# Kernel tuning notes

Measured on AMD Instinct MI355X. Metric: run time of the kernel, lower is better.

The kernel has to match this reference:

```python
import jax, jax.numpy as jnp
import numpy as np

N_NODES = 100000
N_EDGES = 1600000
D_IN = 256
D_OUT = 128


def setup_inputs() -> dict:
    key = jax.random.key(0)
    k1, k2, k3, k4, k5, k6 = jax.random.split(key, 6)
    x = jax.random.normal(k1, (N_NODES, D_IN), dtype=jnp.float32)
    src = jax.random.randint(k2, (N_EDGES,), 0, N_NODES, dtype=jnp.int64)
    dst = jnp.sort(jax.random.randint(k3, (N_EDGES,), 0, N_NODES, dtype=jnp.int64))
    w = jax.random.uniform(k4, (N_EDGES,), dtype=jnp.float32)
    # nn.Linear(input_size, output_size): weight [out, in], bias [out]
    bound = 1.0 / np.sqrt(D_IN)
    W = jax.random.uniform(k5, (D_OUT, D_IN), dtype=jnp.float32, minval=-bound, maxval=bound)
    b = jax.random.uniform(k6, (D_OUT,), dtype=jnp.float32, minval=-bound, maxval=bound)
    return {"x": x, "src": src, "dst": dst, "w": w, "W": W, "b": b}


def reference(x, src, dst, w, W, b):
    # h = linear(x)
    h = jnp.einsum("ni,oi->no", x, W) + b  # [N, D_OUT]
    # u_mul_e: message m_e = h[src_e] * w_e ; sum: out[v] = sum_{e: dst_e=v} m_e
    msgs = h[src] * w[:, None]  # [E, D_OUT]
    out = jax.ops.segment_sum(msgs, dst, num_segments=N_NODES)
    return out
```

## Files before the change

kernel.cpp:

```cpp
#include <hip/hip_runtime.h>

#define N_NODES 100000
#define N_EDGES 1600000
#define D_IN    256
#define D_OUT   128

typedef __attribute__((ext_vector_type(8))) short          bf16x8;
typedef __attribute__((ext_vector_type(8))) unsigned short ushort8;
typedef __attribute__((ext_vector_type(4))) float          f32x4;

__device__ inline unsigned short f2bf(float f) {
  union { float f; unsigned u; } v; v.f = f;
  unsigned r = v.u + 0x7fffu + ((v.u >> 16) & 1u);
  return (unsigned short)(r >> 16);
}
__device__ inline float bf2f(unsigned short u) {
  union { unsigned u; float f; } v; v.u = ((unsigned)u) << 16;
  return v.f;
}

__global__ __launch_bounds__(256) void gcn_packW_kernel(
    const float* __restrict__ W, unsigned short* __restrict__ Wp) {
  int f = blockIdx.x * blockDim.x + threadIdx.x;
  if (f >= 4096) return;
  int n = f >> 9, s = (f >> 6) & 7, lane = f & 63;
  int col = n * 16 + (lane & 15);
  int k0  = s * 32 + (lane >> 4) * 8;
#pragma unroll
  for (int j = 0; j < 8; ++j)
    Wp[f * 8 + j] = f2bf(W[col * D_IN + k0 + j]);
}

__global__ __launch_bounds__(256) void gcn_linear_mfma_kernel(
    const float* __restrict__ x, const unsigned short* __restrict__ Wp,
    const float* __restrict__ b, unsigned short* __restrict__ h) {
  const int lane = threadIdx.x & 63;
  const int wv   = threadIdx.x >> 6;
  const int r0   = blockIdx.x * 64 + wv * 16;

  int arow = r0 + (lane & 15);
  arow = arow < N_NODES ? arow : N_NODES - 1;
  const int kg = (lane >> 4) * 8;
  const float* xrow = x + (size_t)arow * D_IN + kg;

  f32x4 acc[8];
#pragma unroll
  for (int n = 0; n < 8; ++n) acc[n] = (f32x4){0.f, 0.f, 0.f, 0.f};

#pragma unroll
  for (int s = 0; s < 8; ++s) {
    float4 a0 = *(const float4*)(xrow + s * 32);
    float4 a1 = *(const float4*)(xrow + s * 32 + 4);
    bf16x8 af;
    af[0] = (short)f2bf(a0.x); af[1] = (short)f2bf(a0.y);
    af[2] = (short)f2bf(a0.z); af[3] = (short)f2bf(a0.w);
    af[4] = (short)f2bf(a1.x); af[5] = (short)f2bf(a1.y);
    af[6] = (short)f2bf(a1.z); af[7] = (short)f2bf(a1.w);
#pragma unroll
    for (int n = 0; n < 8; ++n) {
      bf16x8 bfrag = *(const bf16x8*)(Wp + ((size_t)((n * 8 + s) * 64 + lane) * 8));
      acc[n] = __builtin_amdgcn_mfma_f32_16x16x32_bf16(af, bfrag, acc[n], 0, 0, 0);
    }
  }

  const int orow0 = r0 + (lane >> 4) * 4;
  const int col0  = lane & 15;
#pragma unroll
  for (int n = 0; n < 8; ++n) {
    const int col = n * 16 + col0;
    const float bias = b[col];
#pragma unroll
    for (int i = 0; i < 4; ++i) {
      const int row = orow0 + i;
      if (row < N_NODES)
        h[(size_t)row * D_OUT + col] = f2bf(acc[n][i] + bias);
    }
  }
}

__global__ __launch_bounds__(256) void gcn_rowptr_kernel(
    const int* __restrict__ dst, int* __restrict__ row_ptr) {
  int v = blockIdx.x * blockDim.x + threadIdx.x;
  if (v > N_NODES) return;
  int lo = 0, hi = N_EDGES;
  while (lo < hi) {
    int mid = (lo + hi) >> 1;
    if (dst[mid] < v) lo = mid + 1; else hi = mid;
  }
  row_ptr[v] = lo;
}

__global__ __launch_bounds__(256) void gcn_agg_kernel(
    const unsigned short* __restrict__ h, const int* __restrict__ src,
    const float* __restrict__ w, const int* __restrict__ rp,
    float* __restrict__ out) {
  const int node = (blockIdx.x << 2) + (threadIdx.x >> 6);
  if (node >= N_NODES) return;
  const int lane = threadIdx.x & 63;
  const int g  = lane >> 4;
  const int dg = (lane & 15) << 3;

  const int s = rp[node], e = rp[node + 1];
  float acc[8];
#pragma unroll
  for (int j = 0; j < 8; ++j) acc[j] = 0.f;

  for (int i = s + g; i < e; i += 4) {
    const int   sv = src[i];
    const float wv = w[i];
    ushort8 hv = *(const ushort8*)(h + (size_t)sv * D_OUT + dg);
#pragma unroll
    for (int j = 0; j < 8; ++j) acc[j] += bf2f(hv[j]) * wv;
  }
#pragma unroll
  for (int j = 0; j < 8; ++j) acc[j] += __shfl_xor(acc[j], 16);
#pragma unroll
  for (int j = 0; j < 8; ++j) acc[j] += __shfl_xor(acc[j], 32);

  if (g == 0) {
    float4 o0 = {acc[0], acc[1], acc[2], acc[3]};
    float4 o1 = {acc[4], acc[5], acc[6], acc[7]};
    float* op = out + (size_t)node * D_OUT + dg;
    *(float4*)(op)     = o0;
    *(float4*)(op + 4) = o1;
  }
}

extern "C" void kernel_launch(void* const* d_in, const int* in_sizes, int n_in,
                              void* d_out, int out_size, void* d_ws, size_t ws_size,
                              hipStream_t stream) {
  const float* x   = (const float*)d_in[0];
  const int*   src = (const int*)d_in[1];
  const int*   dst = (const int*)d_in[2];
  const float* w   = (const float*)d_in[3];
  const float* W   = (const float*)d_in[4];
  const float* b   = (const float*)d_in[5];
  float* out = (float*)d_out;

  unsigned short* Wp = (unsigned short*)d_ws;
  unsigned short* h  = (unsigned short*)((char*)d_ws + 65536);
  int* row_ptr = (int*)((char*)d_ws + 65536 + (size_t)N_NODES * D_OUT * sizeof(unsigned short));

  gcn_packW_kernel<<<16, 256, 0, stream>>>(W, Wp);
  gcn_linear_mfma_kernel<<<(N_NODES + 63) / 64, 256, 0, stream>>>(x, Wp, b, h);
  gcn_rowptr_kernel<<<(N_NODES + 1 + 255) / 256, 256, 0, stream>>>(dst, row_ptr);
  gcn_agg_kernel<<<N_NODES / 4, 256, 0, stream>>>(h, src, w, row_ptr, out);
}
```

Measured before the change: 126.6 us.

## Store h in column-chunked layout and split aggregation across eight feature chunks

The linear kernel now writes h as eight 16-column chunks, each a contiguous [N_NODES,16] bf16 array, and stages the packed W in shared memory using 512-thread blocks. The aggregation kernel launches eight times as many blocks, each handling one 16-feature chunk per node with 16 edges processed in parallel per wave. Each chunk is 3.2 MB, so gathers within a chunk should hit cache more often. The cost is reading src, w and row_ptr eight times and doing more shuffle reductions, with short 8-byte gathers per lane.

```diff
diff --git a/kernel.cpp b/kernel.cpp
--- a/kernel.cpp
+++ b/kernel.cpp
@@ -7,6 +7,7 @@
 
 typedef __attribute__((ext_vector_type(8))) short          bf16x8;
 typedef __attribute__((ext_vector_type(8))) unsigned short ushort8;
+typedef __attribute__((ext_vector_type(4))) unsigned short ushort4_t;
 typedef __attribute__((ext_vector_type(4))) float          f32x4;
 
 __device__ inline unsigned short f2bf(float f) {
@@ -31,12 +32,21 @@
     Wp[f * 8 + j] = f2bf(W[col * D_IN + k0 + j]);
 }
 
-__global__ __launch_bounds__(256) void gcn_linear_mfma_kernel(
+__global__ __launch_bounds__(512) void gcn_linear_mfma_kernel(
     const float* __restrict__ x, const unsigned short* __restrict__ Wp,
-    const float* __restrict__ b, unsigned short* __restrict__ h) {
-  const int lane = threadIdx.x & 63;
-  const int wv   = threadIdx.x >> 6;
-  const int r0   = blockIdx.x * 64 + wv * 16;
+    const float* __restrict__ b, unsigned short* __restrict__ hT) {
+  __shared__ unsigned short lW[32768];
+  const int tid  = threadIdx.x;
+  const int lane = tid & 63;
+  const int wid  = tid >> 6;
+  const int r0   = blockIdx.x * 128 + wid * 16;
+
+#pragma unroll
+  for (int i = 0; i < 8; ++i) {
+    int idx = i * 512 + tid;
+    *(ushort8*)(&lW[idx * 8]) = *(const ushort8*)(Wp + (size_t)idx * 8);
+  }
+  __syncthreads();
 
   int arow = r0 + (lane & 15);
   arow = arow < N_NODES ? arow : N_NODES - 1;
@@ -58,22 +68,22 @@
     af[6] = (short)f2bf(a1.z); af[7] = (short)f2bf(a1.w);
 #pragma unroll
     for (int n = 0; n < 8; ++n) {
-      bf16x8 bfrag = *(const bf16x8*)(Wp + ((size_t)((n * 8 + s) * 64 + lane) * 8));
+      bf16x8 bfrag = *(const bf16x8*)(&lW[(size_t)((n * 8 + s) * 64 + lane) * 8]);
       acc[n] = __builtin_amdgcn_mfma_f32_16x16x32_bf16(af, bfrag, acc[n], 0, 0, 0);
     }
   }
 
-  const int orow0 = r0 + (lane >> 4) * 4;
-  const int col0  = lane & 15;
+  const int col0 = lane & 15;
+  const int q4   = (lane >> 4) * 4;
 #pragma unroll
   for (int n = 0; n < 8; ++n) {
-    const int col = n * 16 + col0;
-    const float bias = b[col];
+    const float bias = b[n * 16 + col0];
+    unsigned short* hc = hT + (size_t)n * N_NODES * 16;
 #pragma unroll
     for (int i = 0; i < 4; ++i) {
-      const int row = orow0 + i;
+      const int row = r0 + q4 + i;
       if (row < N_NODES)
-        h[(size_t)row * D_OUT + col] = f2bf(acc[n][i] + bias);
+        hc[(size_t)row * 16 + col0] = f2bf(acc[n][i] + bias);
     }
   }
 }
@@ -91,38 +101,42 @@
 }
 
 __global__ __launch_bounds__(256) void gcn_agg_kernel(
-    const unsigned short* __restrict__ h, const int* __restrict__ src,
+    const unsigned short* __restrict__ hT, const int* __restrict__ src,
     const float* __restrict__ w, const int* __restrict__ rp,
     float* __restrict__ out) {
-  const int node = (blockIdx.x << 2) + (threadIdx.x >> 6);
+  const int chunk = blockIdx.x & 7;
+  const int node  = ((blockIdx.x >> 3) << 2) + (threadIdx.x >> 6);
   if (node >= N_NODES) return;
   const int lane = threadIdx.x & 63;
-  const int g  = lane >> 4;
-  const int dg = (lane & 15) << 3;
+  const int slot = lane >> 2;
+  const int q    = lane & 3;
+  const unsigned short* hc = hT + (size_t)chunk * N_NODES * 16;
 
   const int s = rp[node], e = rp[node + 1];
-  float acc[8];
+  float acc[4] = {0.f, 0.f, 0.f, 0.f};
+
+  for (int base = s; base < e; base += 16) {
+    const int  i = base + slot;
+    const bool valid = (i < e);
+    const int  ic = valid ? i : s;
+    const int   sv = src[ic];
+    const float wv = valid ? w[ic] : 0.f;
+    ushort4_t hv = *(const ushort4_t*)(hc + (size_t)sv * 16 + (q << 2));
 #pragma unroll
-  for (int j = 0; j < 8; ++j) acc[j] = 0.f;
+    for (int k = 0; k < 4; ++k) acc[k] += bf2f(hv[k]) * wv;
+  }
 
-  for (int i = s + g; i < e; i += 4) {
-    const int   sv = src[i];
-    const float wv = w[i];
-    ushort8 hv = *(const ushort8*)(h + (size_t)sv * D_OUT + dg);
 #pragma unroll
-    for (int j = 0; j < 8; ++j) acc[j] += bf2f(hv[j]) * wv;
+  for (int k = 0; k < 4; ++k) {
+    acc[k] += __shfl_xor(acc[k], 4);
+    acc[k] += __shfl_xor(acc[k], 8);
+    acc[k] += __shfl_xor(acc[k], 16);
+    acc[k] += __shfl_xor(acc[k], 32);
   }
-#pragma unroll
-  for (int j = 0; j < 8; ++j) acc[j] += __shfl_xor(acc[j], 16);
-#pragma unroll
-  for (int j = 0; j < 8; ++j) acc[j] += __shfl_xor(acc[j], 32);
 
-  if (g == 0) {
-    float4 o0 = {acc[0], acc[1], acc[2], acc[3]};
-    float4 o1 = {acc[4], acc[5], acc[6], acc[7]};
-    float* op = out + (size_t)node * D_OUT + dg;
-    *(float4*)(op)     = o0;
-    *(float4*)(op + 4) = o1;
+  if (slot == 0) {
+    float4 o = {acc[0], acc[1], acc[2], acc[3]};
+    *(float4*)(out + (size_t)node * D_OUT + chunk * 16 + (q << 2)) = o;
   }
 }
 
@@ -138,11 +152,11 @@
   float* out = (float*)d_out;
 
   unsigned short* Wp = (unsigned short*)d_ws;
-  unsigned short* h  = (unsigned short*)((char*)d_ws + 65536);
+  unsigned short* hT = (unsigned short*)((char*)d_ws + 65536);
   int* row_ptr = (int*)((char*)d_ws + 65536 + (size_t)N_NODES * D_OUT * sizeof(unsigned short));
 
   gcn_packW_kernel<<<16, 256, 0, stream>>>(W, Wp);
-  gcn_linear_mfma_kernel<<<(N_NODES + 63) / 64, 256, 0, stream>>>(x, Wp, b, h);
+  gcn_linear_mfma_kernel<<<(N_NODES + 127) / 128, 512, 0, stream>>>(x, Wp, b, hT);
   gcn_rowptr_kernel<<<(N_NODES + 1 + 255) / 256, 256, 0, stream>>>(dst, row_ptr);
-  gcn_agg_kernel<<<N_NODES / 4, 256, 0, stream>>>(h, src, w, row_ptr, out);
+  gcn_agg_kernel<<<8 * (N_NODES / 4), 256, 0, stream>>>(hT, src, w, row_ptr, out);
 }
```

Result: slower. 246.6 us (+94.8%).

## Stage packed W in LDS for linear and batch 4 gathers per lane in aggregation

Applied to the files above, without the earlier changes.

The linear kernel now runs 512-thread blocks covering 128 rows and first copies the whole 64KB packed bf16 W into shared memory, so MFMA B fragments come from LDS rather than global/L2. The aggregation loop has each 16-lane group take four consecutive edges per step and issue four independent row gathers before accumulating, which raises memory-level parallelism. The rowptr launch is moved ahead of the linear launch. The 64KB LDS footprint per block limits occupancy and adds a preload per block, and the unrolled gathers raise register pressure.

```diff
diff --git a/kernel.cpp b/kernel.cpp
--- a/kernel.cpp
+++ b/kernel.cpp
@@ -31,12 +31,21 @@
     Wp[f * 8 + j] = f2bf(W[col * D_IN + k0 + j]);
 }
 
-__global__ __launch_bounds__(256) void gcn_linear_mfma_kernel(
+__global__ __launch_bounds__(512) void gcn_linear_mfma_kernel(
     const float* __restrict__ x, const unsigned short* __restrict__ Wp,
     const float* __restrict__ b, unsigned short* __restrict__ h) {
-  const int lane = threadIdx.x & 63;
-  const int wv   = threadIdx.x >> 6;
-  const int r0   = blockIdx.x * 64 + wv * 16;
+  __shared__ unsigned short lW[32768];
+  const int tid  = threadIdx.x;
+  const int lane = tid & 63;
+  const int wid  = tid >> 6;
+  const int r0   = blockIdx.x * 128 + wid * 16;
+
+#pragma unroll
+  for (int i = 0; i < 8; ++i) {
+    int idx = i * 512 + tid;
+    *(ushort8*)(&lW[idx * 8]) = *(const ushort8*)(Wp + (size_t)idx * 8);
+  }
+  __syncthreads();
 
   int arow = r0 + (lane & 15);
   arow = arow < N_NODES ? arow : N_NODES - 1;
@@ -58,20 +67,20 @@
     af[6] = (short)f2bf(a1.z); af[7] = (short)f2bf(a1.w);
 #pragma unroll
     for (int n = 0; n < 8; ++n) {
-      bf16x8 bfrag = *(const bf16x8*)(Wp + ((size_t)((n * 8 + s) * 64 + lane) * 8));
+      bf16x8 bfrag = *(const bf16x8*)(&lW[(size_t)((n * 8 + s) * 64 + lane) * 8]);
       acc[n] = __builtin_amdgcn_mfma_f32_16x16x32_bf16(af, bfrag, acc[n], 0, 0, 0);
     }
   }
 
-  const int orow0 = r0 + (lane >> 4) * 4;
-  const int col0  = lane & 15;
+  const int col0 = lane & 15;
+  const int q4   = (lane >> 4) * 4;
 #pragma unroll
   for (int n = 0; n < 8; ++n) {
     const int col = n * 16 + col0;
     const float bias = b[col];
 #pragma unroll
     for (int i = 0; i < 4; ++i) {
-      const int row = orow0 + i;
+      const int row = r0 + q4 + i;
       if (row < N_NODES)
         h[(size_t)row * D_OUT + col] = f2bf(acc[n][i] + bias);
     }
@@ -105,13 +114,31 @@
 #pragma unroll
   for (int j = 0; j < 8; ++j) acc[j] = 0.f;
 
-  for (int i = s + g; i < e; i += 4) {
-    const int   sv = src[i];
-    const float wv = w[i];
-    ushort8 hv = *(const ushort8*)(h + (size_t)sv * D_OUT + dg);
+  for (int base = s; base < e; base += 16) {
+    const int i0 = base + (g << 2);
+    if (i0 < e) {
+      int   sv[4];
+      float wv[4];
 #pragma unroll
-    for (int j = 0; j < 8; ++j) acc[j] += bf2f(hv[j]) * wv;
+      for (int j = 0; j < 4; ++j) {
+        int  i = i0 + j;
+        bool valid = (i < e);
+        int  ic = valid ? i : i0;
+        sv[j] = src[ic];
+        wv[j] = valid ? w[ic] : 0.f;
+      }
+      ushort8 hv[4];
+#pragma unroll
+      for (int j = 0; j < 4; ++j)
+        hv[j] = *(const ushort8*)(h + (size_t)sv[j] * D_OUT + dg);
+#pragma unroll
+      for (int j = 0; j < 4; ++j)
+#pragma unroll
+        for (int k = 0; k < 8; ++k)
+          acc[k] += bf2f(hv[j][k]) * wv[j];
+    }
   }
+
 #pragma unroll
   for (int j = 0; j < 8; ++j) acc[j] += __shfl_xor(acc[j], 16);
 #pragma unroll
@@ -142,7 +169,7 @@
   int* row_ptr = (int*)((char*)d_ws + 65536 + (size_t)N_NODES * D_OUT * sizeof(unsigned short));
 
   gcn_packW_kernel<<<16, 256, 0, stream>>>(W, Wp);
-  gcn_linear_mfma_kernel<<<(N_NODES + 63) / 64, 256, 0, stream>>>(x, Wp, b, h);
   gcn_rowptr_kernel<<<(N_NODES + 1 + 255) / 256, 256, 0, stream>>>(dst, row_ptr);
+  gcn_linear_mfma_kernel<<<(N_NODES + 127) / 128, 512, 0, stream>>>(x, Wp, b, h);
   gcn_agg_kernel<<<N_NODES / 4, 256, 0, stream>>>(h, src, w, row_ptr, out);
 }
```

Result: faster. 110.7 us (-12.5%).
